# Kernel optimization log

Measured on AMD Instinct MI355X. Metric: run time of the kernel, lower is better.

The kernel has to match this reference:

```python
import jax, jax.numpy as jnp
import numpy as np

H_DIM = 1024
N_HEADS = 16
HEAD_D = H_DIM // N_HEADS  # 64


def setup_inputs() -> dict:
    key = jax.random.key(0)
    ks = jax.random.split(key, 10)
    B, T, C = 2, 2048, H_DIM
    init = 1.0 / np.sqrt(C)  # lecun_normal-scale stand-in
    src = jax.random.normal(ks[0], (B, T, C), dtype=jnp.float32)
    mask = jnp.ones((B, T), dtype=jnp.float32)  # unused when causal
    Wq = jax.random.normal(ks[1], (C, H_DIM), dtype=jnp.float32) * init
    Wk = jax.random.normal(ks[2], (C, H_DIM), dtype=jnp.float32) * init
    Wv = jax.random.normal(ks[3], (C, H_DIM), dtype=jnp.float32) * init
    Wo = jax.random.normal(ks[4], (H_DIM, H_DIM), dtype=jnp.float32) * init
    bq = jnp.zeros((H_DIM,), jnp.float32)
    bk = jnp.zeros((H_DIM,), jnp.float32)
    bv = jnp.zeros((H_DIM,), jnp.float32)
    bo = jnp.zeros((H_DIM,), jnp.float32)
    return {"src": src, "mask": mask, "Wq": Wq, "bq": bq, "Wk": Wk, "bk": bk,
            "Wv": Wv, "bv": bv, "Wo": Wo, "bo": bo}


def reference(src, mask, Wq, bq, Wk, bk, Wv, bv, Wo, bo):
    # MaskedCausalAttention forward, deterministic=True (dropout = identity),
    # use_causal_mask=True.
    B, T, C = src.shape
    N, D = N_HEADS, HEAD_D
    # q,k,v: [B, N, T, D]
    q = (src @ Wq + bq).reshape(B, T, N, D).transpose(0, 2, 1, 3)
    k = (src @ Wk + bk).reshape(B, T, N, D).transpose(0, 2, 1, 3)
    v = (src @ Wv + bv).reshape(B, T, N, D).transpose(0, 2, 1, 3)
    # scores: [B, N, T, T]
    scores = jnp.einsum('bntd,bnsd->bnts', q, k) / jnp.sqrt(jnp.float32(D))
    causal = jnp.tril(jnp.ones((T, T), dtype=bool))[None, None]
    scores = jnp.where(causal, scores, -jnp.inf)
    probs = jax.nn.softmax(scores, axis=-1)
    attn = jnp.einsum('bnts,bnsd->bntd', probs, v)  # [B, N, T, D]
    attn = attn.transpose(0, 2, 1, 3).reshape(B, T, N * D)
    return attn @ Wo + bo
```

## Files before the change

### kernel.cpp

```cpp
#include <hip/hip_runtime.h>
#include <hip/hip_bf16.h>

typedef __hip_bfloat16 bf16;
typedef __attribute__((ext_vector_type(8))) short short8;
typedef __attribute__((ext_vector_type(4))) float f32x4;

#define BATCH 2
#define SEQ   2048
#define HDIM  1024
#define NHEAD 16
#define DHEAD 64
#define MROWS (BATCH*SEQ)

#define QSCALE 0.18033688f
#define EXP2F(x) __builtin_amdgcn_exp2f(x)

static __device__ __forceinline__ short f2bs(float x) {
    __hip_bfloat16 h = (__hip_bfloat16)x;
    return *reinterpret_cast<short*>(&h);
}
static __device__ __forceinline__ unsigned int pk2(float a, float b) {
    __hip_bfloat162 h = __float22bfloat162_rn(make_float2(a, b));
    return *reinterpret_cast<unsigned int*>(&h);
}

static __device__ __forceinline__ void gload16(const void* g, void* l) {
    __builtin_amdgcn_global_load_lds(
        (const __attribute__((address_space(1))) unsigned int*)g,
        (__attribute__((address_space(3))) unsigned int*)l, 16, 0, 0);
}

__global__ __launch_bounds__(256) void prep1(const float* __restrict__ src,
        const float* __restrict__ Wq, const float* __restrict__ Wk,
        const float* __restrict__ Wv, const float* __restrict__ Wo,
        short* __restrict__ Sb, short* __restrict__ WT,
        short* __restrict__ WoT)
{
    __shared__ float t[64][65];
    const int bx = blockIdx.x, tid = threadIdx.x;
    if (bx < 4096) {
        int i = bx * 256 + tid;
        float4 v = ((const float4*)src)[i];
        ushort4 o;
        o.x = (unsigned short)f2bs(v.x);
        o.y = (unsigned short)f2bs(v.y);
        o.z = (unsigned short)f2bs(v.z);
        o.w = (unsigned short)f2bs(v.w);
        ((ushort4*)Sb)[i] = o;
        return;
    }
    const int tb = bx - 4096;
    const int wsel = tb >> 8;
    const float* W = (wsel == 0) ? Wq : (wsel == 1) ? Wk : (wsel == 2) ? Wv : Wo;
    short* dst = (wsel < 3) ? WT : WoT;
    const int roff = (wsel < 3) ? wsel * 1024 : 0;
    const int t8 = tb & 255;
    const int n0 = (t8 & 15) * 64, k0 = (t8 >> 4) * 64;
#pragma unroll
    for (int i = 0; i < 16; i++) {
        int idx = tid + i * 256, r = idx >> 6, c = idx & 63;
        t[r][c] = W[(size_t)(k0 + r) * HDIM + n0 + c];
    }
    __syncthreads();
#pragma unroll
    for (int i = 0; i < 16; i++) {
        int idx = tid + i * 256, c = idx >> 6, r = idx & 63;
        dst[(size_t)(roff + n0 + c) * HDIM + k0 + r] = f2bs(t[r][c]);
    }
}

__global__ __launch_bounds__(512, 2) void gemm_qkv(const short* __restrict__ A,
        const short* __restrict__ Bt,
        const float* __restrict__ bq, const float* __restrict__ bk,
        const float* __restrict__ bv,
        short* __restrict__ Qout, short* __restrict__ Kout,
        short* __restrict__ Vtout)
{
    __shared__ short SM[3 * 12288];
    const int tid = threadIdx.x, lane = tid & 63, w = tid >> 6;
    const int quad = lane >> 4, l15 = lane & 15;
    const int m0 = blockIdx.y * 256, n0 = blockIdx.x * 128;
    const int wr = w >> 1, wc = w & 1;

    const short* gsrc[3];
    short* ldst[3];
#pragma unroll
    for (int i = 0; i < 3; i++) {
        int u = w * 3 + i;
        if (u < 16) {
            gsrc[i] = A + (size_t)(m0 + u * 16 + l15) * HDIM + quad * 8;
            ldst[i] = &SM[u * 512];
        } else {
            int v = u - 16;
            gsrc[i] = Bt + (size_t)(n0 + v * 16 + l15) * HDIM + quad * 8;
            ldst[i] = &SM[8192 + v * 512];
        }
    }

    f32x4 acc[4][4];
#pragma unroll
    for (int i = 0; i < 4; i++)
#pragma unroll
        for (int j = 0; j < 4; j++) acc[i][j] = (f32x4){0.f, 0.f, 0.f, 0.f};

#pragma unroll
    for (int i = 0; i < 3; i++) { gload16(gsrc[i], ldst[i]); gsrc[i] += 32; }
#pragma unroll
    for (int i = 0; i < 3; i++) { gload16(gsrc[i], ldst[i] + 12288); gsrc[i] += 32; }

    for (int kk = 0; kk < 32; ++kk) {
        if (kk < 30) {
            const int nb = ((kk + 2) % 3) * 12288;
#pragma unroll
            for (int i = 0; i < 3; i++) { gload16(gsrc[i], ldst[i] + nb); gsrc[i] += 32; }
            asm volatile("s_waitcnt vmcnt(6)" ::: "memory");
        } else if (kk == 30) {
            asm volatile("s_waitcnt vmcnt(3)" ::: "memory");
        } else {
            asm volatile("s_waitcnt vmcnt(0)" ::: "memory");
        }
        __builtin_amdgcn_s_barrier();
        const short* Asb = &SM[(kk % 3) * 12288];
        const short* Bsb = Asb + 8192;
        short8 af[4], bfr[4];
#pragma unroll
        for (int mi = 0; mi < 4; mi++)
            af[mi] = *(const short8*)&Asb[(wr * 4 + mi) * 512 + lane * 8];
#pragma unroll
        for (int ni = 0; ni < 4; ni++)
            bfr[ni] = *(const short8*)&Bsb[(wc * 4 + ni) * 512 + lane * 8];
#pragma unroll
        for (int mi = 0; mi < 4; mi++)
#pragma unroll
            for (int ni = 0; ni < 4; ni++)
                acc[mi][ni] = __builtin_amdgcn_mfma_f32_16x16x32_bf16(
                                  af[mi], bfr[ni], acc[mi][ni], 0, 0, 0);
        __builtin_amdgcn_s_barrier();
    }

    const int region = n0 >> 10;
    if (region < 2) {
        const float* bias = region ? bk : bq;
        const float oscale = region ? 1.0f : QSCALE;
        short* C = region ? Kout : Qout;
#pragma unroll
        for (int mi = 0; mi < 4; mi++) {
            int mB = m0 + (wr * 4 + mi) * 16 + quad * 4;
#pragma unroll
            for (int ni = 0; ni < 4; ni++) {
                int nl = (n0 + (wc * 4 + ni) * 16 + l15) & 1023;
                float bb = bias[nl];
#pragma unroll
                for (int r = 0; r < 4; r++)
                    C[(size_t)(mB + r) * HDIM + nl] =
                        f2bs((acc[mi][ni][r] + bb) * oscale);
            }
        }
    } else {
#pragma unroll
        for (int mi = 0; mi < 4; mi++) {
            int mB = m0 + (wr * 4 + mi) * 16 + quad * 4;
            int bb = mB >> 11, t = mB & 2047;
#pragma unroll
            for (int ni = 0; ni < 4; ni++) {
                int n = n0 + (wc * 4 + ni) * 16 + l15;
                int h = (n >> 6) & 15, d = n & 63;
                float bvv = bv[n & 1023];
                size_t base = ((size_t)((bb * NHEAD + h) * DHEAD + d)) * SEQ + t;
                ushort4 pk;
                pk.x = (unsigned short)f2bs(acc[mi][ni][0] + bvv);
                pk.y = (unsigned short)f2bs(acc[mi][ni][1] + bvv);
                pk.z = (unsigned short)f2bs(acc[mi][ni][2] + bvv);
                pk.w = (unsigned short)f2bs(acc[mi][ni][3] + bvv);
                *(ushort4*)(Vtout + base) = pk;
            }
        }
    }
}

__global__ __launch_bounds__(256) void attn_mfma(const short* __restrict__ Qb,
        const short* __restrict__ Kb, const short* __restrict__ Vt,
        short* __restrict__ Ab)
{
    __shared__ short SMEM[29184];
    const int tid = threadIdx.x, lane = tid & 63, w = tid >> 6;
    const int quad = lane >> 4, l15 = lane & 15;
    const int L = blockIdx.x;

    const int pair = (L & 7) + 8 * ((L >> 3) & 3);
    const int strip = 31 - (L >> 5);
    const int b = pair >> 4, head = pair & 15;

    const short* Kbh = Kb + (size_t)b * SEQ * HDIM + head * DHEAD;
    const short* Vth = Vt + (size_t)(b * NHEAD + head) * DHEAD * SEQ;
    short* Pw = SMEM + 24576 + w * 1152;

    const int qbase = strip * 64;
    const int qr = qbase + w * 16 + l15;

    const short* qptr = Qb + (size_t)(b * SEQ + qr) * HDIM + head * DHEAD + quad * 8;
    short8 bq0 = *(const short8*)qptr;
    short8 bq1 = *(const short8*)(qptr + 32);

    const short* gp[4];
    int stp[4], ldo[4];
#pragma unroll
    for (int i = 0; i < 4; i++) {
        int u = w * 4 + i;
        if (u < 8) {
            int t = u >> 1, h = u & 1;
            gp[i] = Kbh + (size_t)(t * 16 + l15) * HDIM + h * 32 + quad * 8;
            stp[i] = 64 * HDIM;
        } else {
            int c = u - 8, dt = c >> 1, kh = c & 1;
            gp[i] = Vth + (size_t)(dt * 16 + l15) * SEQ + kh * 32 + quad * 8;
            stp[i] = 64;
        }
        ldo[i] = u * 512;
    }

    f32x4 o[4];
#pragma unroll
    for (int dt = 0; dt < 4; dt++) o[dt] = (f32x4){0.f, 0.f, 0.f, 0.f};
    float psum = 0.f;

#pragma unroll
    for (int i = 0; i < 4; i++) { gload16(gp[i], &SMEM[ldo[i]]); gp[i] += stp[i]; }
    if (strip >= 1) {
#pragma unroll
        for (int i = 0; i < 4; i++) { gload16(gp[i], &SMEM[8192 + ldo[i]]); gp[i] += stp[i]; }
    }

    for (int it = 0; it <= strip; ++it) {
        short* Ks = &SMEM[(it % 3) * 8192];
        short* Vs = Ks + 4096;

        if (it + 2 <= strip) {
            short* nb = &SMEM[((it + 2) % 3) * 8192];
#pragma unroll
            for (int i = 0; i < 4; i++) { gload16(gp[i], nb + ldo[i]); gp[i] += stp[i]; }
            asm volatile("s_waitcnt vmcnt(8)" ::: "memory");
        } else if (it + 1 <= strip) {
            asm volatile("s_waitcnt vmcnt(4)" ::: "memory");
        } else {
            asm volatile("s_waitcnt vmcnt(0)" ::: "memory");
        }
        __builtin_amdgcn_s_barrier();
        const int s0 = it * 64;
        f32x4 sv[4];
        __builtin_amdgcn_s_setprio(1);
#pragma unroll
        for (int t = 0; t < 4; t++) {
            sv[t] = (f32x4){0.f, 0.f, 0.f, 0.f};
            short8 k0 = *(const short8*)&Ks[(t * 2) * 512 + lane * 8];
            short8 k1 = *(const short8*)&Ks[(t * 2 + 1) * 512 + lane * 8];
            sv[t] = __builtin_amdgcn_mfma_f32_16x16x32_bf16(k0, bq0, sv[t], 0, 0, 0);
            sv[t] = __builtin_amdgcn_mfma_f32_16x16x32_bf16(k1, bq1, sv[t], 0, 0, 0);
        }
        __builtin_amdgcn_s_setprio(0);

        float p[16];
        if (it == strip) {
#pragma unroll
            for (int t = 0; t < 4; t++)
#pragma unroll
                for (int r = 0; r < 4; r++) {
                    int key = s0 + t * 16 + quad * 4 + r;
                    p[t * 4 + r] = (key <= qr) ? EXP2F(sv[t][r]) : 0.f;
                }
        } else {
#pragma unroll
            for (int t = 0; t < 4; t++)
#pragma unroll
                for (int r = 0; r < 4; r++)
                    p[t * 4 + r] = EXP2F(sv[t][r]);
        }
#pragma unroll
        for (int i = 0; i < 16; i++) psum += p[i];

#pragma unroll
        for (int t = 0; t < 4; t++) {
            uint2 u2;
            u2.x = pk2(p[t * 4],     p[t * 4 + 1]);
            u2.y = pk2(p[t * 4 + 2], p[t * 4 + 3]);
            *(uint2*)&Pw[l15 * 72 + t * 16 + quad * 4] = u2;
        }
        short8 bp0 = *(const short8*)&Pw[l15 * 72 + quad * 8];
        short8 bp1 = *(const short8*)&Pw[l15 * 72 + 32 + quad * 8];

        __builtin_amdgcn_s_setprio(1);
#pragma unroll
        for (int dt = 0; dt < 4; dt++) {
            short8 av0 = *(const short8*)&Vs[(dt * 2) * 512 + lane * 8];
            short8 av1 = *(const short8*)&Vs[(dt * 2 + 1) * 512 + lane * 8];
            o[dt] = __builtin_amdgcn_mfma_f32_16x16x32_bf16(av0, bp0, o[dt], 0, 0, 0);
            o[dt] = __builtin_amdgcn_mfma_f32_16x16x32_bf16(av1, bp1, o[dt], 0, 0, 0);
        }
        __builtin_amdgcn_s_setprio(0);
        __builtin_amdgcn_s_barrier();
    }

    float lrow = psum + __shfl_xor(psum, 16);
    lrow += __shfl_xor(lrow, 32);
    const float inv = 1.f / lrow;

    const size_t obase = (size_t)(b * SEQ + qr) * HDIM + head * DHEAD;
#pragma unroll
    for (int dt = 0; dt < 4; dt++) {
        uint2 u2;
        u2.x = pk2(o[dt][0] * inv, o[dt][1] * inv);
        u2.y = pk2(o[dt][2] * inv, o[dt][3] * inv);
        *(uint2*)&Ab[obase + dt * 16 + quad * 4] = u2;
    }
}

__global__ __launch_bounds__(256) void gemm_o(const short* __restrict__ A,
        const short* __restrict__ Bt, const float* __restrict__ bo,
        float* __restrict__ Out)
{
    __shared__ short SM[3 * 6144];
    const int tid = threadIdx.x, lane = tid & 63, w = tid >> 6;
    const int quad = lane >> 4, l15 = lane & 15;
    const int m0 = blockIdx.y * 64, n0 = blockIdx.x * 128;
    const int wr = w >> 1, wc = w & 1;

    const short* gsrc[3];
    short* ldst[3];
#pragma unroll
    for (int i = 0; i < 3; i++) {
        int u = w * 3 + i;
        if (u < 4) {
            gsrc[i] = A + (size_t)(m0 + u * 16 + l15) * HDIM + quad * 8;
            ldst[i] = &SM[u * 512];
        } else {
            int v = u - 4;
            gsrc[i] = Bt + (size_t)(n0 + v * 16 + l15) * HDIM + quad * 8;
            ldst[i] = &SM[2048 + v * 512];
        }
    }

    f32x4 acc[2][4];
#pragma unroll
    for (int i = 0; i < 2; i++)
#pragma unroll
        for (int j = 0; j < 4; j++) acc[i][j] = (f32x4){0.f, 0.f, 0.f, 0.f};

#pragma unroll
    for (int i = 0; i < 3; i++) { gload16(gsrc[i], ldst[i]); gsrc[i] += 32; }
#pragma unroll
    for (int i = 0; i < 3; i++) { gload16(gsrc[i], ldst[i] + 6144); gsrc[i] += 32; }

    for (int kk = 0; kk < 32; ++kk) {
        if (kk < 30) {
            const int nb = ((kk + 2) % 3) * 6144;
#pragma unroll
            for (int i = 0; i < 3; i++) { gload16(gsrc[i], ldst[i] + nb); gsrc[i] += 32; }
            asm volatile("s_waitcnt vmcnt(6)" ::: "memory");
        } else if (kk == 30) {
            asm volatile("s_waitcnt vmcnt(3)" ::: "memory");
        } else {
            asm volatile("s_waitcnt vmcnt(0)" ::: "memory");
        }
        __builtin_amdgcn_s_barrier();

        const short* Asb = &SM[(kk % 3) * 6144];
        const short* Bsb = Asb + 2048;
        short8 af[2], bfr[4];
#pragma unroll
        for (int mi = 0; mi < 2; mi++)
            af[mi] = *(const short8*)&Asb[(wr * 2 + mi) * 512 + lane * 8];
#pragma unroll
        for (int ni = 0; ni < 4; ni++)
            bfr[ni] = *(const short8*)&Bsb[(wc * 4 + ni) * 512 + lane * 8];
#pragma unroll
        for (int mi = 0; mi < 2; mi++)
#pragma unroll
            for (int ni = 0; ni < 4; ni++)
                acc[mi][ni] = __builtin_amdgcn_mfma_f32_16x16x32_bf16(
                                  af[mi], bfr[ni], acc[mi][ni], 0, 0, 0);
        __builtin_amdgcn_s_barrier();
    }

#pragma unroll
    for (int mi = 0; mi < 2; mi++) {
        int mB = m0 + (wr * 2 + mi) * 16 + quad * 4;
#pragma unroll
        for (int ni = 0; ni < 4; ni++) {
            int n = n0 + (wc * 4 + ni) * 16 + l15;
            float bb = bo[n];
#pragma unroll
            for (int r = 0; r < 4; r++)
                Out[(size_t)(mB + r) * HDIM + n] = acc[mi][ni][r] + bb;
        }
    }
}

extern "C" void kernel_launch(void* const* d_in, const int* in_sizes, int n_in,
                              void* d_out, int out_size, void* d_ws, size_t ws_size,
                              hipStream_t stream)
{
    const float* src = (const float*)d_in[0];
    const float* Wq = (const float*)d_in[2];
    const float* bq = (const float*)d_in[3];
    const float* Wk = (const float*)d_in[4];
    const float* bk = (const float*)d_in[5];
    const float* Wv = (const float*)d_in[6];
    const float* bv = (const float*)d_in[7];
    const float* Wo = (const float*)d_in[8];
    const float* bo = (const float*)d_in[9];
    float* out = (float*)d_out;

    short* Sb   = (short*)d_ws;
    short* Qb   = Sb + (size_t)MROWS * HDIM;
    short* Kb   = Qb + (size_t)MROWS * HDIM;
    short* Vt   = Kb + (size_t)MROWS * HDIM;
    short* WoT  = Vt + (size_t)MROWS * HDIM;
    short* WT   = (short*)d_out;
    short* Ab   = Qb;

    prep1<<<dim3(4096 + 1024), dim3(256), 0, stream>>>(src, Wq, Wk, Wv, Wo, Sb, WT, WoT);

    gemm_qkv<<<dim3(24, 16), dim3(512), 0, stream>>>(Sb, WT, bq, bk, bv, Qb, Kb, Vt);

    attn_mfma<<<dim3(1024), dim3(256), 0, stream>>>(Qb, Kb, Vt, Ab);

    gemm_o<<<dim3(8, 64), dim3(256), 0, stream>>>(Ab, WoT, bo, out);
}
```

Measured before the change: 212.3 us.

## Enlarge QKV GEMM tile to 256x256 with K=64 double-buffered phased pipeline

Rewrites the fused QKV projection GEMM to use 256x256 output tiles (8 waves, each 64x128) with a K-step of 64, double-buffered in LDS. Global loads for the next stage are split across four sub-phases that are interleaved with MFMA groups, and s_setprio raises wave priority around the MFMA bursts. This is meant to raise arithmetic intensity and hide load latency, at the cost of 128KB of LDS (one block per CU), more accumulator registers, and half as many blocks (192), which may leave part of the device idle.

```diff
diff --git a/kernel.cpp b/kernel.cpp
--- a/kernel.cpp
+++ b/kernel.cpp
@@ -76,79 +76,102 @@
         short* __restrict__ Qout, short* __restrict__ Kout,
         short* __restrict__ Vtout)
 {
-    __shared__ short SM[3 * 12288];
+    __shared__ short SM[2][32768];
     const int tid = threadIdx.x, lane = tid & 63, w = tid >> 6;
     const int quad = lane >> 4, l15 = lane & 15;
-    const int m0 = blockIdx.y * 256, n0 = blockIdx.x * 128;
+    const int m0 = blockIdx.y * 256, n0 = blockIdx.x * 256;
     const int wr = w >> 1, wc = w & 1;
 
-    const short* gsrc[3];
-    short* ldst[3];
-#pragma unroll
-    for (int i = 0; i < 3; i++) {
-        int u = w * 3 + i;
-        if (u < 16) {
-            gsrc[i] = A + (size_t)(m0 + u * 16 + l15) * HDIM + quad * 8;
-            ldst[i] = &SM[u * 512];
-        } else {
-            int v = u - 16;
-            gsrc[i] = Bt + (size_t)(n0 + v * 16 + l15) * HDIM + quad * 8;
-            ldst[i] = &SM[8192 + v * 512];
-        }
-    }
-
-    f32x4 acc[4][4];
+    const short* gp[4][2];
+    int lo[4][2];
+#pragma unroll
+    for (int g = 0; g < 4; g++)
+#pragma unroll
+        for (int i = 0; i < 2; i++) {
+            if (g < 2) {
+                int u = g * 16 + w * 2 + i;
+                gp[g][i] = A + (size_t)(m0 + (u >> 1) * 16 + l15) * HDIM
+                             + (u & 1) * 32 + quad * 8;
+                lo[g][i] = u * 512;
+            } else {
+                int j = w * 2 + i;
+                int v = (g == 2 ? 0 : 8) + j + (j >= 8 ? 8 : 0);
+                gp[g][i] = Bt + (size_t)(n0 + (v >> 1) * 16 + l15) * HDIM
+                              + (v & 1) * 32 + quad * 8;
+                lo[g][i] = 16384 + v * 512;
+            }
+        }
+
+    f32x4 acc[4][8];
 #pragma unroll
     for (int i = 0; i < 4; i++)
 #pragma unroll
-        for (int j = 0; j < 4; j++) acc[i][j] = (f32x4){0.f, 0.f, 0.f, 0.f};
-
-#pragma unroll
-    for (int i = 0; i < 3; i++) { gload16(gsrc[i], ldst[i]); gsrc[i] += 32; }
-#pragma unroll
-    for (int i = 0; i < 3; i++) { gload16(gsrc[i], ldst[i] + 12288); gsrc[i] += 32; }
-
-    for (int kk = 0; kk < 32; ++kk) {
-        if (kk < 30) {
-            const int nb = ((kk + 2) % 3) * 12288;
-#pragma unroll
-            for (int i = 0; i < 3; i++) { gload16(gsrc[i], ldst[i] + nb); gsrc[i] += 32; }
-            asm volatile("s_waitcnt vmcnt(6)" ::: "memory");
-        } else if (kk == 30) {
-            asm volatile("s_waitcnt vmcnt(3)" ::: "memory");
-        } else {
-            asm volatile("s_waitcnt vmcnt(0)" ::: "memory");
-        }
-        __builtin_amdgcn_s_barrier();
-        const short* Asb = &SM[(kk % 3) * 12288];
-        const short* Bsb = Asb + 8192;
-        short8 af[4], bfr[4];
-#pragma unroll
-        for (int mi = 0; mi < 4; mi++)
-            af[mi] = *(const short8*)&Asb[(wr * 4 + mi) * 512 + lane * 8];
-#pragma unroll
-        for (int ni = 0; ni < 4; ni++)
-            bfr[ni] = *(const short8*)&Bsb[(wc * 4 + ni) * 512 + lane * 8];
-#pragma unroll
-        for (int mi = 0; mi < 4; mi++)
-#pragma unroll
-            for (int ni = 0; ni < 4; ni++)
-                acc[mi][ni] = __builtin_amdgcn_mfma_f32_16x16x32_bf16(
-                                  af[mi], bfr[ni], acc[mi][ni], 0, 0, 0);
-        __builtin_amdgcn_s_barrier();
-    }
-
-    const int region = n0 >> 10;
+        for (int j = 0; j < 8; j++) acc[i][j] = (f32x4){0.f, 0.f, 0.f, 0.f};
+
+#pragma unroll
+    for (int g = 0; g < 4; g++)
+#pragma unroll
+        for (int i = 0; i < 2; i++) { gload16(gp[g][i], &SM[0][lo[g][i]]); gp[g][i] += 64; }
+    asm volatile("s_waitcnt vmcnt(2)" ::: "memory");
+    __builtin_amdgcn_s_barrier();
+
+    short8 af[4][2];
+    for (int t = 0; t < 16; ++t) {
+        const short* Tb = SM[t & 1];
+        short* Sn = SM[(t + 1) & 1];
+#pragma unroll
+        for (int p = 0; p < 4; ++p) {
+            if (p == 0) {
+#pragma unroll
+                for (int mi = 0; mi < 4; mi++)
+#pragma unroll
+                    for (int kh = 0; kh < 2; kh++)
+                        af[mi][kh] = *(const short8*)
+                            &Tb[((wr * 4 + mi) * 2 + kh) * 512 + lane * 8];
+            }
+            short8 bfp[2][2];
+#pragma unroll
+            for (int n2 = 0; n2 < 2; n2++)
+#pragma unroll
+                for (int kh = 0; kh < 2; kh++)
+                    bfp[n2][kh] = *(const short8*)
+                        &Tb[16384 + ((wc * 8 + p * 2 + n2) * 2 + kh) * 512 + lane * 8];
+
+            if (t < 15) {
+                gload16(gp[p][0], Sn + lo[p][0]); gp[p][0] += 64;
+                gload16(gp[p][1], Sn + lo[p][1]); gp[p][1] += 64;
+                if (p == 1) asm volatile("s_waitcnt vmcnt(4)" ::: "memory");
+                if (p == 3) asm volatile("s_waitcnt vmcnt(2)" ::: "memory");
+            } else {
+                if (p == 1) asm volatile("s_waitcnt vmcnt(0)" ::: "memory");
+            }
+            __builtin_amdgcn_s_barrier();
+            asm volatile("s_waitcnt lgkmcnt(0)" ::: "memory");
+            __builtin_amdgcn_s_setprio(1);
+#pragma unroll
+            for (int n2 = 0; n2 < 2; n2++)
+#pragma unroll
+                for (int mi = 0; mi < 4; mi++)
+#pragma unroll
+                    for (int kh = 0; kh < 2; kh++)
+                        acc[mi][p * 2 + n2] = __builtin_amdgcn_mfma_f32_16x16x32_bf16(
+                            af[mi][kh], bfp[n2][kh], acc[mi][p * 2 + n2], 0, 0, 0);
+            __builtin_amdgcn_s_setprio(0);
+            __builtin_amdgcn_s_barrier();
+        }
+    }
+
+    const int region = blockIdx.x >> 2;
     if (region < 2) {
         const float* bias = region ? bk : bq;
         const float oscale = region ? 1.0f : QSCALE;
         short* C = region ? Kout : Qout;
 #pragma unroll
         for (int mi = 0; mi < 4; mi++) {
-            int mB = m0 + (wr * 4 + mi) * 16 + quad * 4;
-#pragma unroll
-            for (int ni = 0; ni < 4; ni++) {
-                int nl = (n0 + (wc * 4 + ni) * 16 + l15) & 1023;
+            int mB = m0 + wr * 64 + mi * 16 + quad * 4;
+#pragma unroll
+            for (int ni = 0; ni < 8; ni++) {
+                int nl = (n0 + (wc * 8 + ni) * 16 + l15) & 1023;
                 float bb = bias[nl];
 #pragma unroll
                 for (int r = 0; r < 4; r++)
@@ -159,14 +182,14 @@
     } else {
 #pragma unroll
         for (int mi = 0; mi < 4; mi++) {
-            int mB = m0 + (wr * 4 + mi) * 16 + quad * 4;
-            int bb = mB >> 11, t = mB & 2047;
-#pragma unroll
-            for (int ni = 0; ni < 4; ni++) {
-                int n = n0 + (wc * 4 + ni) * 16 + l15;
+            int mB = m0 + wr * 64 + mi * 16 + quad * 4;
+            int bb = mB >> 11, tt = mB & 2047;
+#pragma unroll
+            for (int ni = 0; ni < 8; ni++) {
+                int n = n0 + (wc * 8 + ni) * 16 + l15;
                 int h = (n >> 6) & 15, d = n & 63;
                 float bvv = bv[n & 1023];
-                size_t base = ((size_t)((bb * NHEAD + h) * DHEAD + d)) * SEQ + t;
+                size_t base = ((size_t)((bb * NHEAD + h) * DHEAD + d)) * SEQ + tt;
                 ushort4 pk;
                 pk.x = (unsigned short)f2bs(acc[mi][ni][0] + bvv);
                 pk.y = (unsigned short)f2bs(acc[mi][ni][1] + bvv);
@@ -420,7 +443,7 @@
 
     prep1<<<dim3(4096 + 1024), dim3(256), 0, stream>>>(src, Wq, Wk, Wv, Wo, Sb, WT, WoT);
 
-    gemm_qkv<<<dim3(24, 16), dim3(512), 0, stream>>>(Sb, WT, bq, bk, bv, Qb, Kb, Vt);
+    gemm_qkv<<<dim3(12, 16), dim3(512), 0, stream>>>(Sb, WT, bq, bk, bv, Qb, Kb, Vt);
 
     attn_mfma<<<dim3(1024), dim3(256), 0, stream>>>(Qb, Kb, Vt, Ab);
 
```

Measured after the change: 206.7 us. 2.6% less time.
